# Performance work log

Hardware: AMD Instinct MI355X
Metric: run time of the kernel (lower is better)

## Reference

```python
import jax, jax.numpy as jnp
import numpy as np

N_NODES = 50000
N_EDGES = 800000


def _sage(x, src, dst, Wl, bl, Wr):
    # mean-aggregate neighbor features (messages flow src -> dst), then linear
    msg = x[src]                                              # [E, d_in]
    s = jax.ops.segment_sum(msg, dst, num_segments=N_NODES)   # [N, d_in]
    cnt = jax.ops.segment_sum(jnp.ones((src.shape[0],), x.dtype), dst,
                              num_segments=N_NODES)           # [N]
    agg = s / jnp.maximum(cnt, 1.0)[:, None]
    return agg @ Wl.T + bl + x @ Wr.T


def setup_inputs() -> dict:
    key = jax.random.key(0)
    ks = jax.random.split(key, 10)
    d_in, h = 128, 64
    def w(k, o, i):
        return jax.random.normal(k, (o, i), jnp.float32) * (1.0 / np.sqrt(i))
    return {
        "x": jax.random.normal(ks[0], (N_NODES, d_in), jnp.float32),
        "edge_index": jax.random.randint(ks[1], (2, N_EDGES), 0, N_NODES, jnp.int64),
        "Wl1": w(ks[2], h, d_in), "bl1": jnp.zeros((h,), jnp.float32), "Wr1": w(ks[3], h, d_in),
        "Wl2": w(ks[4], 2 * h, h), "bl2": jnp.zeros((2 * h,), jnp.float32), "Wr2": w(ks[5], 2 * h, h),
        "Wl3": w(ks[6], 2 * h, 2 * h), "bl3": jnp.zeros((2 * h,), jnp.float32), "Wr3": w(ks[7], 2 * h, 2 * h),
        "Wl4": w(ks[8], h, 2 * h), "bl4": jnp.zeros((h,), jnp.float32), "Wr4": w(ks[9], h, 2 * h),
    }


def reference(x, edge_index, Wl1, bl1, Wr1, Wl2, bl2, Wr2, Wl3, bl3, Wr3, Wl4, bl4, Wr4):
    src, dst = edge_index[0], edge_index[1]
    h = jax.nn.relu(_sage(x, src, dst, Wl1, bl1, Wr1))
    h = jax.nn.relu(_sage(h, src, dst, Wl2, bl2, Wr2))
    h = jax.nn.relu(_sage(h, src, dst, Wl3, bl3, Wr3))
    h = _sage(h, src, dst, Wl4, bl4, Wr4)
    return h
```

## Files before the change

kernel.cpp:

```cpp
#include <hip/hip_runtime.h>

#define NN 50000
#define NE 800000
#define GB 391
#define NBUK 196
#define PB 128
#define CH 6250
#define HLEN (NBUK * PB)
#define SAB (HLEN / 256)

typedef __attribute__((ext_vector_type(8))) short short8v;
typedef __attribute__((ext_vector_type(4))) float float4v;

__device__ __forceinline__ int uni(int v) { return __builtin_amdgcn_readfirstlane(v); }
__device__ __forceinline__ unsigned short f2bf(float f) {
    unsigned u = __float_as_uint(f);
    return (unsigned short)((u + 0x7FFFu + ((u >> 16) & 1u)) >> 16);
}
__device__ __forceinline__ float bf2f(unsigned short h) {
    return __uint_as_float(((unsigned)h) << 16);
}

__global__ __launch_bounds__(256) void hist_kernel(const int* __restrict__ dst,
                                                   int* __restrict__ H) {
    __shared__ int h[NBUK];
    const int t = threadIdx.x;
    const int b = blockIdx.x;
    if (t < NBUK) h[t] = 0;
    __syncthreads();
    const int e0 = b * CH;
    for (int i = t; i < CH; i += 256) {
        int e = e0 + i;
        if (e < NE) atomicAdd(&h[dst[e] >> 8], 1);
    }
    __syncthreads();
    if (t < NBUK) H[t * PB + b] = h[t];
}

__global__ __launch_bounds__(256) void scanA_kernel(const int* __restrict__ a,
                                                    int* __restrict__ part) {
    __shared__ int red[256];
    const int t = threadIdx.x;
    red[t] = a[blockIdx.x * 256 + t];
    __syncthreads();
#pragma unroll
    for (int d = 128; d > 0; d >>= 1) {
        if (t < d) red[t] += red[t + d];
        __syncthreads();
    }
    if (t == 0) part[blockIdx.x] = red[0];
}

__global__ __launch_bounds__(128) void scanB_kernel(int* __restrict__ part) {
    __shared__ int ps[128];
    const int t = threadIdx.x;
    ps[t] = (t < SAB) ? part[t] : 0;
    __syncthreads();
#pragma unroll
    for (int d = 1; d < 128; d <<= 1) {
        int v = (t >= d) ? ps[t - d] : 0;
        __syncthreads();
        ps[t] += v;
        __syncthreads();
    }
    if (t < SAB) part[t] = (t == 0) ? 0 : ps[t - 1];
}

__global__ __launch_bounds__(256) void scanC_kernel(int* __restrict__ a,
                                                    const int* __restrict__ part) {
    __shared__ int ps[256];
    const int t = threadIdx.x;
    const int i = blockIdx.x * 256 + t;
    const int c = a[i];
    ps[t] = c;
    __syncthreads();
#pragma unroll
    for (int d = 1; d < 256; d <<= 1) {
        int v = (t >= d) ? ps[t - d] : 0;
        __syncthreads();
        ps[t] += v;
        __syncthreads();
    }
    a[i] = part[blockIdx.x] + ps[t] - c;
}

__global__ __launch_bounds__(256) void partition_kernel(const int* __restrict__ src,
                                                        const int* __restrict__ dst,
                                                        const int* __restrict__ Hs,
                                                        unsigned* __restrict__ tmp) {
    __shared__ int cur[NBUK];
    const int t = threadIdx.x;
    const int b = blockIdx.x;
    if (t < NBUK) cur[t] = Hs[t * PB + b];
    __syncthreads();
    const int e0 = b * CH;
    for (int i = t; i < CH; i += 256) {
        int e = e0 + i;
        if (e < NE) {
            const int d = dst[e];
            const int k = d >> 8;
            const int pos = atomicAdd(&cur[k], 1);
            tmp[pos] = (unsigned)src[e] | ((unsigned)(d & 255) << 16);
        }
    }
}

__global__ __launch_bounds__(256) void finalize_kernel(const unsigned* __restrict__ tmp,
                                                       const int* __restrict__ Hs,
                                                       int* __restrict__ off,
                                                       int* __restrict__ cnt,
                                                       float* __restrict__ inv,
                                                       int* __restrict__ srcs) {
    __shared__ int hist[256];
    __shared__ int ps[256];
    __shared__ int cur[256];
    const int t = threadIdx.x;
    const int k = blockIdx.x;
    const int s0 = Hs[k * PB];
    const int end = (k == NBUK - 1) ? NE : Hs[(k + 1) * PB];
    const int m = end - s0;
    hist[t] = 0;
    __syncthreads();
    for (int i = t; i < m; i += 256) {
        atomicAdd(&hist[(tmp[s0 + i] >> 16) & 255], 1);
    }
    __syncthreads();
    const int c = hist[t];
    ps[t] = c;
    __syncthreads();
#pragma unroll
    for (int d = 1; d < 256; d <<= 1) {
        int v = (t >= d) ? ps[t - d] : 0;
        __syncthreads();
        ps[t] += v;
        __syncthreads();
    }
    const int ex = ps[t] - c;
    const int node = k * 256 + t;
    if (node < NN) {
        off[node] = s0 + ex;
        cnt[node] = c;
        inv[node] = 1.0f / (float)max(c, 1);
    }
    cur[t] = s0 + ex;
    __syncthreads();
    for (int i = t; i < m; i += 256) {
        const unsigned u = tmp[s0 + i];
        const int p = atomicAdd(&cur[(u >> 16) & 255], 1);
        srcs[p] = (int)(u & 0xFFFFu);
    }
}

template<int D, int MODE, int DUALB>
__global__ __launch_bounds__(256) void gather_kernel(
    const unsigned short* __restrict__ yb, int ys, const int* __restrict__ srcs,
    const int* __restrict__ off, const int* __restrict__ cnt,
    const float* __restrict__ inv, const float* __restrict__ pre, int ps,
    float* __restrict__ out, int os, unsigned short* __restrict__ outb) {
    const int w = (blockIdx.x * blockDim.x + threadIdx.x) >> 6;
    const int lane = threadIdx.x & 63;
    if (w >= NN) return;
    const int o = uni(off[w]);
    const int n = uni(cnt[w]);
    const int h = lane >> 5;
    const int l = lane & 31;

    float a0 = 0.0f, a1 = 0.0f, a2 = 0.0f, a3 = 0.0f;
    int i = 0;
    for (; i + 8 <= n; i += 8) {
        int e0 = srcs[o + i + h];
        int e1 = srcs[o + i + 2 + h];
        int e2 = srcs[o + i + 4 + h];
        int e3 = srcs[o + i + 6 + h];
        if constexpr (D == 64) {
            const ushort2 v0 = *reinterpret_cast<const ushort2*>(&yb[(size_t)e0 * ys + 2 * l]);
            const ushort2 v1 = *reinterpret_cast<const ushort2*>(&yb[(size_t)e1 * ys + 2 * l]);
            const ushort2 v2 = *reinterpret_cast<const ushort2*>(&yb[(size_t)e2 * ys + 2 * l]);
            const ushort2 v3 = *reinterpret_cast<const ushort2*>(&yb[(size_t)e3 * ys + 2 * l]);
            a0 += bf2f(v0.x) + bf2f(v1.x) + bf2f(v2.x) + bf2f(v3.x);
            a1 += bf2f(v0.y) + bf2f(v1.y) + bf2f(v2.y) + bf2f(v3.y);
        } else {
            const ushort4 v0 = *reinterpret_cast<const ushort4*>(&yb[(size_t)e0 * ys + 4 * l]);
            const ushort4 v1 = *reinterpret_cast<const ushort4*>(&yb[(size_t)e1 * ys + 4 * l]);
            const ushort4 v2 = *reinterpret_cast<const ushort4*>(&yb[(size_t)e2 * ys + 4 * l]);
            const ushort4 v3 = *reinterpret_cast<const ushort4*>(&yb[(size_t)e3 * ys + 4 * l]);
            a0 += bf2f(v0.x) + bf2f(v1.x) + bf2f(v2.x) + bf2f(v3.x);
            a1 += bf2f(v0.y) + bf2f(v1.y) + bf2f(v2.y) + bf2f(v3.y);
            a2 += bf2f(v0.z) + bf2f(v1.z) + bf2f(v2.z) + bf2f(v3.z);
            a3 += bf2f(v0.w) + bf2f(v1.w) + bf2f(v2.w) + bf2f(v3.w);
        }
    }
    for (; i + 2 <= n; i += 2) {
        int e = srcs[o + i + h];
        if constexpr (D == 64) {
            const ushort2 v = *reinterpret_cast<const ushort2*>(&yb[(size_t)e * ys + 2 * l]);
            a0 += bf2f(v.x);
            a1 += bf2f(v.y);
        } else {
            const ushort4 v = *reinterpret_cast<const ushort4*>(&yb[(size_t)e * ys + 4 * l]);
            a0 += bf2f(v.x); a1 += bf2f(v.y); a2 += bf2f(v.z); a3 += bf2f(v.w);
        }
    }
    if (i < n && h == 0) {
        int e = srcs[o + i];
        if constexpr (D == 64) {
            const ushort2 v = *reinterpret_cast<const ushort2*>(&yb[(size_t)e * ys + 2 * l]);
            a0 += bf2f(v.x);
            a1 += bf2f(v.y);
        } else {
            const ushort4 v = *reinterpret_cast<const ushort4*>(&yb[(size_t)e * ys + 4 * l]);
            a0 += bf2f(v.x); a1 += bf2f(v.y); a2 += bf2f(v.z); a3 += bf2f(v.w);
        }
    }
    a0 += __shfl_xor(a0, 32, 64);
    a1 += __shfl_xor(a1, 32, 64);
    if constexpr (D == 128) {
        a2 += __shfl_xor(a2, 32, 64);
        a3 += __shfl_xor(a3, 32, 64);
    }
    if (h != 0) return;

    const float iv = inv[w];
    if constexpr (D == 64) {
        float r0 = a0 * iv, r1 = a1 * iv;
        if constexpr (MODE != 0) {
            const float2 pv = *reinterpret_cast<const float2*>(&pre[(size_t)w * ps + 2 * l]);
            r0 += pv.x; r1 += pv.y;
        }
        if constexpr (MODE == 1) { r0 = fmaxf(r0, 0.0f); r1 = fmaxf(r1, 0.0f); }
        float2 sv = {r0, r1};
        *reinterpret_cast<float2*>(&out[(size_t)w * os + 2 * l]) = sv;
        if constexpr (DUALB) {
            ushort2 bv = {f2bf(r0), f2bf(r1)};
            *reinterpret_cast<ushort2*>(&outb[(size_t)w * 64 + 2 * l]) = bv;
        }
    } else {
        float r0 = a0 * iv, r1 = a1 * iv, r2 = a2 * iv, r3 = a3 * iv;
        if constexpr (MODE != 0) {
            const float4 pv = *reinterpret_cast<const float4*>(&pre[(size_t)w * ps + 4 * l]);
            r0 += pv.x; r1 += pv.y; r2 += pv.z; r3 += pv.w;
        }
        if constexpr (MODE == 1) {
            r0 = fmaxf(r0, 0.0f); r1 = fmaxf(r1, 0.0f);
            r2 = fmaxf(r2, 0.0f); r3 = fmaxf(r3, 0.0f);
        }
        float4 sv = {r0, r1, r2, r3};
        *reinterpret_cast<float4*>(&out[(size_t)w * os + 4 * l]) = sv;
    }
}

struct WSrc { const float* p[8]; };

__global__ __launch_bounds__(256) void wplanes_kernel(WSrc S,
                                                      unsigned short* __restrict__ ph,
                                                      unsigned short* __restrict__ pl) {
    const int e = blockIdx.x * 256 + threadIdx.x;
    const int seg = blockIdx.y;
    const int row = e >> 7, k = e & 127;
    float x;
    switch (seg) {
        case 0:  x = (row < 64) ? S.p[0][row * 128 + k] : S.p[1][(row - 64) * 128 + k]; break;
        case 1:  x = (k < 64)   ? S.p[2][row * 64 + k]  : S.p[3][row * 64 + (k - 64)];  break;
        case 2:  x = S.p[4][e]; break;
        case 3:  x = S.p[5][e]; break;
        default: x = (row < 64) ? S.p[6][row * 128 + k] : S.p[7][(row - 64) * 128 + k]; break;
    }
    const unsigned u = __float_as_uint(x);
    const float lo = x - __uint_as_float(u & 0xFFFF0000u);
    const int o = seg * 16384 + e;
    ph[o] = (unsigned short)(u >> 16);
    pl[o] = (unsigned short)(__float_as_uint(lo) >> 16);
}

__global__ __launch_bounds__(256) void gemm_mfma(
    const float* __restrict__ in,
    const unsigned short* __restrict__ Bh, const unsigned short* __restrict__ Bl,
    float* __restrict__ out0, const float* __restrict__ bias0, int os0, int obf0,
    float* __restrict__ out1, const float* __restrict__ bias1, int os1, int obf1,
    int relu) {
    const int t = threadIdx.x;
    const int lane = t & 63;
    const int wid = t >> 6;
    const int wn = wid & 1;
    const int wc = wid >> 1;
    const int l15 = lane & 15;
    const int lk = lane >> 4;
    const int nb = (int)blockIdx.x * 128 + wn * 64;

    float* const outp = wc ? out1 : out0;
    const float* const biasp = wc ? bias1 : bias0;
    const int os = wc ? os1 : os0;
    const int obf = wc ? obf1 : obf0;
    const unsigned short* const Bhp = Bh + (size_t)(wc * 64) * 128;
    const unsigned short* const Blp = Bl + (size_t)(wc * 64) * 128;
    const ptrdiff_t dlo = Blp - Bhp;

    float4v acc[4][4];
#pragma unroll
    for (int mi = 0; mi < 4; ++mi)
#pragma unroll
        for (int ci = 0; ci < 4; ++ci) acc[mi][ci] = (float4v)0.0f;

    const float* arow[4];
#pragma unroll
    for (int mi = 0; mi < 4; ++mi) {
        int r = nb + mi * 16 + l15;
        if (r > NN - 1) r = NN - 1;
        arow[mi] = in + (size_t)r * 128;
    }
    const unsigned short* brow[4];
#pragma unroll
    for (int ci = 0; ci < 4; ++ci) brow[ci] = Bhp + (size_t)(ci * 16 + l15) * 128;

    for (int ks = 0; ks < 4; ++ks) {
        const int ko = ks * 32 + lk * 8;
        short8v Ah[4], Al[4];
#pragma unroll
        for (int mi = 0; mi < 4; ++mi) {
            const float4v v0 = *reinterpret_cast<const float4v*>(arow[mi] + ko);
            const float4v v1 = *reinterpret_cast<const float4v*>(arow[mi] + ko + 4);
            float xv[8] = {v0.x, v0.y, v0.z, v0.w, v1.x, v1.y, v1.z, v1.w};
            union { unsigned u[4]; short8v s; } H, L;
#pragma unroll
            for (int q = 0; q < 4; ++q) {
                const unsigned u0 = __float_as_uint(xv[2 * q]);
                const unsigned u1 = __float_as_uint(xv[2 * q + 1]);
                const float l0 = xv[2 * q]     - __uint_as_float(u0 & 0xFFFF0000u);
                const float l1 = xv[2 * q + 1] - __uint_as_float(u1 & 0xFFFF0000u);
                H.u[q] = (u1 & 0xFFFF0000u) | (u0 >> 16);
                L.u[q] = (__float_as_uint(l1) & 0xFFFF0000u) | (__float_as_uint(l0) >> 16);
            }
            Ah[mi] = H.s;
            Al[mi] = L.s;
        }
        short8v Bhf[4], Blf[4];
#pragma unroll
        for (int ci = 0; ci < 4; ++ci) {
            Bhf[ci] = *reinterpret_cast<const short8v*>(brow[ci] + ko);
            Blf[ci] = *reinterpret_cast<const short8v*>(brow[ci] + dlo + ko);
        }
#pragma unroll
        for (int mi = 0; mi < 4; ++mi)
#pragma unroll
            for (int ci = 0; ci < 4; ++ci) {
                acc[mi][ci] = __builtin_amdgcn_mfma_f32_16x16x32_bf16(Ah[mi], Bhf[ci], acc[mi][ci], 0, 0, 0);
                acc[mi][ci] = __builtin_amdgcn_mfma_f32_16x16x32_bf16(Ah[mi], Blf[ci], acc[mi][ci], 0, 0, 0);
                acc[mi][ci] = __builtin_amdgcn_mfma_f32_16x16x32_bf16(Al[mi], Bhf[ci], acc[mi][ci], 0, 0, 0);
            }
    }

#pragma unroll
    for (int ci = 0; ci < 4; ++ci) {
        const int c = ci * 16 + l15;
        const float b = biasp ? biasp[c] : 0.0f;
#pragma unroll
        for (int mi = 0; mi < 4; ++mi) {
#pragma unroll
            for (int j = 0; j < 4; ++j) {
                const int r = nb + mi * 16 + lk * 4 + j;
                if (r < NN) {
                    float v = acc[mi][ci][j] + b;
                    if (relu) v = fmaxf(v, 0.0f);
                    if (obf) ((unsigned short*)outp)[(size_t)r * os + c] = f2bf(v);
                    else outp[(size_t)r * os + c] = v;
                }
            }
        }
    }
}

extern "C" void kernel_launch(void* const* d_in, const int* in_sizes, int n_in,
                              void* d_out, int out_size, void* d_ws, size_t ws_size,
                              hipStream_t stream) {
    const float* x   = (const float*)d_in[0];
    const int*   eix = (const int*)d_in[1];
    const float* Wl1 = (const float*)d_in[2];
    const float* bl1 = (const float*)d_in[3];
    const float* Wr1 = (const float*)d_in[4];
    const float* Wl2 = (const float*)d_in[5];
    const float* bl2 = (const float*)d_in[6];
    const float* Wr2 = (const float*)d_in[7];
    const float* Wl3 = (const float*)d_in[8];
    const float* bl3 = (const float*)d_in[9];
    const float* Wr3 = (const float*)d_in[10];
    const float* Wl4 = (const float*)d_in[11];
    const float* bl4 = (const float*)d_in[12];
    const float* Wr4 = (const float*)d_in[13];
    float* out = (float*)d_out;

    const int* src = eix;
    const int* dst = eix + NE;

    char* ws = (char*)d_ws;
    int*   cnt  = (int*)ws;
    int*   off  = cnt + NN;
    float* inv  = (float*)(off + NN);
    int*   Hs   = (int*)(inv + NN);
    int*   part = Hs + HLEN;
    int*   srcs = part + 256;
    unsigned short* ph = (unsigned short*)(srcs + NE);
    unsigned short* pl = ph + 81920;
    unsigned short* XB1 = pl + 81920;
    unsigned short* H1B = XB1 + (size_t)NN * 64;
    unsigned short* G3B = XB1;
    float* HCAT = (float*)(XB1 + (size_t)NN * 128);
    float* H2   = HCAT + (size_t)NN * 128;
    float* HPRE = H2 + (size_t)NN * 128;
    unsigned*       tmp = (unsigned*)HPRE;
    unsigned short* G4B = (unsigned short*)HCAT;

    hist_kernel<<<PB, 256, 0, stream>>>(dst, Hs);
    scanA_kernel<<<SAB, 256, 0, stream>>>(Hs, part);
    scanB_kernel<<<1, 128, 0, stream>>>(part);
    scanC_kernel<<<SAB, 256, 0, stream>>>(Hs, part);
    partition_kernel<<<PB, 256, 0, stream>>>(src, dst, Hs, tmp);
    finalize_kernel<<<NBUK, 256, 0, stream>>>(tmp, Hs, off, cnt, inv, srcs);

    {
        WSrc s;
        s.p[0] = Wl1; s.p[1] = Wr1; s.p[2] = Wl2; s.p[3] = Wr2;
        s.p[4] = Wl3; s.p[5] = Wr3; s.p[6] = Wl4; s.p[7] = Wr4;
        wplanes_kernel<<<dim3(64, 5), 256, 0, stream>>>(s, ph, pl);
    }

    gemm_mfma<<<GB, 256, 0, stream>>>(x, ph, pl,
                                      (float*)XB1, nullptr, 64, 1,
                                      HCAT + 64, bl1, 128, 0, 0);
    gather_kernel<64, 1, 1><<<12500, 256, 0, stream>>>(
        XB1, 64, srcs, off, cnt, inv, HCAT + 64, 128, HCAT + 64, 128, H1B);

    gather_kernel<64, 0, 0><<<12500, 256, 0, stream>>>(
        H1B, 64, srcs, off, cnt, inv, nullptr, 0, HCAT, 128, nullptr);
    gemm_mfma<<<GB, 256, 0, stream>>>(HCAT, ph + 16384, pl + 16384,
                                      H2, bl2, 128, 0,
                                      H2 + 64, bl2 + 64, 128, 0, 1);

    gemm_mfma<<<GB, 256, 0, stream>>>(H2, ph + 2 * 16384, pl + 2 * 16384,
                                      (float*)G3B, nullptr, 128, 1,
                                      (float*)(G3B + 64), nullptr, 128, 1, 0);
    gemm_mfma<<<GB, 256, 0, stream>>>(H2, ph + 3 * 16384, pl + 3 * 16384,
                                      HPRE, bl3, 128, 0,
                                      HPRE + 64, bl3 + 64, 128, 0, 0);
    gather_kernel<128, 1, 0><<<12500, 256, 0, stream>>>(
        G3B, 128, srcs, off, cnt, inv, HPRE, 128, HPRE, 128, nullptr);

    gemm_mfma<<<GB, 256, 0, stream>>>(HPRE, ph + 4 * 16384, pl + 4 * 16384,
                                      (float*)G4B, nullptr, 64, 1,
                                      out, bl4, 64, 0, 0);
    gather_kernel<64, 2, 0><<<12500, 256, 0, stream>>>(
        G4B, 64, srcs, off, cnt, inv, out, 64, out, 64, nullptr);
}
```

Before: 323.9 us.

## Use 16-bit edge indices, nontemporal memory ops, and merge layer-3 GEMM launches

Stores the CSR source index array as 16-bit values to halve index bandwidth in the gather kernels. Adds nontemporal loads and stores across the gather and GEMM kernels to reduce cache pollution. Merges the two layer-3 GEMMs that share an input into a single launch using a 2D grid with per-y argument structs. Nontemporal stores of intermediates that are read right afterwards may lose L2 reuse, and the 16-bit index relies on node count staying below 65536.

```diff
diff --git a/kernel.cpp b/kernel.cpp
--- a/kernel.cpp
+++ b/kernel.cpp
@@ -11,6 +11,8 @@
 
 typedef __attribute__((ext_vector_type(8))) short short8v;
 typedef __attribute__((ext_vector_type(4))) float float4v;
+typedef __attribute__((ext_vector_type(2))) float float2v;
+typedef __attribute__((ext_vector_type(2))) unsigned short ushort2v;
 
 __device__ __forceinline__ int uni(int v) { return __builtin_amdgcn_readfirstlane(v); }
 __device__ __forceinline__ unsigned short f2bf(float f) {
@@ -110,7 +112,7 @@
                                                        int* __restrict__ off,
                                                        int* __restrict__ cnt,
                                                        float* __restrict__ inv,
-                                                       int* __restrict__ srcs) {
+                                                       unsigned short* __restrict__ srcs) {
     __shared__ int hist[256];
     __shared__ int ps[256];
     __shared__ int cur[256];
@@ -147,13 +149,13 @@
     for (int i = t; i < m; i += 256) {
         const unsigned u = tmp[s0 + i];
         const int p = atomicAdd(&cur[(u >> 16) & 255], 1);
-        srcs[p] = (int)(u & 0xFFFFu);
+        srcs[p] = (unsigned short)(u & 0xFFFFu);
     }
 }
 
 template<int D, int MODE, int DUALB>
 __global__ __launch_bounds__(256) void gather_kernel(
-    const unsigned short* __restrict__ yb, int ys, const int* __restrict__ srcs,
+    const unsigned short* __restrict__ yb, int ys, const unsigned short* __restrict__ srcs,
     const int* __restrict__ off, const int* __restrict__ cnt,
     const float* __restrict__ inv, const float* __restrict__ pre, int ps,
     float* __restrict__ out, int os, unsigned short* __restrict__ outb) {
@@ -168,10 +170,10 @@
     float a0 = 0.0f, a1 = 0.0f, a2 = 0.0f, a3 = 0.0f;
     int i = 0;
     for (; i + 8 <= n; i += 8) {
-        int e0 = srcs[o + i + h];
-        int e1 = srcs[o + i + 2 + h];
-        int e2 = srcs[o + i + 4 + h];
-        int e3 = srcs[o + i + 6 + h];
+        int e0 = __builtin_nontemporal_load(&srcs[o + i + h]);
+        int e1 = __builtin_nontemporal_load(&srcs[o + i + 2 + h]);
+        int e2 = __builtin_nontemporal_load(&srcs[o + i + 4 + h]);
+        int e3 = __builtin_nontemporal_load(&srcs[o + i + 6 + h]);
         if constexpr (D == 64) {
             const ushort2 v0 = *reinterpret_cast<const ushort2*>(&yb[(size_t)e0 * ys + 2 * l]);
             const ushort2 v1 = *reinterpret_cast<const ushort2*>(&yb[(size_t)e1 * ys + 2 * l]);
@@ -191,7 +193,7 @@
         }
     }
     for (; i + 2 <= n; i += 2) {
-        int e = srcs[o + i + h];
+        int e = __builtin_nontemporal_load(&srcs[o + i + h]);
         if constexpr (D == 64) {
             const ushort2 v = *reinterpret_cast<const ushort2*>(&yb[(size_t)e * ys + 2 * l]);
             a0 += bf2f(v.x);
@@ -202,7 +204,7 @@
         }
     }
     if (i < n && h == 0) {
-        int e = srcs[o + i];
+        int e = __builtin_nontemporal_load(&srcs[o + i]);
         if constexpr (D == 64) {
             const ushort2 v = *reinterpret_cast<const ushort2*>(&yb[(size_t)e * ys + 2 * l]);
             a0 += bf2f(v.x);
@@ -224,28 +226,30 @@
     if constexpr (D == 64) {
         float r0 = a0 * iv, r1 = a1 * iv;
         if constexpr (MODE != 0) {
-            const float2 pv = *reinterpret_cast<const float2*>(&pre[(size_t)w * ps + 2 * l]);
+            const float2v pv = __builtin_nontemporal_load(
+                reinterpret_cast<const float2v*>(&pre[(size_t)w * ps + 2 * l]));
             r0 += pv.x; r1 += pv.y;
         }
         if constexpr (MODE == 1) { r0 = fmaxf(r0, 0.0f); r1 = fmaxf(r1, 0.0f); }
-        float2 sv = {r0, r1};
-        *reinterpret_cast<float2*>(&out[(size_t)w * os + 2 * l]) = sv;
+        float2v sv = {r0, r1};
+        __builtin_nontemporal_store(sv, reinterpret_cast<float2v*>(&out[(size_t)w * os + 2 * l]));
         if constexpr (DUALB) {
-            ushort2 bv = {f2bf(r0), f2bf(r1)};
-            *reinterpret_cast<ushort2*>(&outb[(size_t)w * 64 + 2 * l]) = bv;
+            ushort2v bv = {f2bf(r0), f2bf(r1)};
+            __builtin_nontemporal_store(bv, reinterpret_cast<ushort2v*>(&outb[(size_t)w * 64 + 2 * l]));
         }
     } else {
         float r0 = a0 * iv, r1 = a1 * iv, r2 = a2 * iv, r3 = a3 * iv;
         if constexpr (MODE != 0) {
-            const float4 pv = *reinterpret_cast<const float4*>(&pre[(size_t)w * ps + 4 * l]);
+            const float4v pv = __builtin_nontemporal_load(
+                reinterpret_cast<const float4v*>(&pre[(size_t)w * ps + 4 * l]));
             r0 += pv.x; r1 += pv.y; r2 += pv.z; r3 += pv.w;
         }
         if constexpr (MODE == 1) {
             r0 = fmaxf(r0, 0.0f); r1 = fmaxf(r1, 0.0f);
             r2 = fmaxf(r2, 0.0f); r3 = fmaxf(r3, 0.0f);
         }
-        float4 sv = {r0, r1, r2, r3};
-        *reinterpret_cast<float4*>(&out[(size_t)w * os + 4 * l]) = sv;
+        float4v sv = {r0, r1, r2, r3};
+        __builtin_nontemporal_store(sv, reinterpret_cast<float4v*>(&out[(size_t)w * os + 4 * l]));
     }
 }
 
@@ -272,12 +276,16 @@
     pl[o] = (unsigned short)(__float_as_uint(lo) >> 16);
 }
 
-__global__ __launch_bounds__(256) void gemm_mfma(
-    const float* __restrict__ in,
-    const unsigned short* __restrict__ Bh, const unsigned short* __restrict__ Bl,
-    float* __restrict__ out0, const float* __restrict__ bias0, int os0, int obf0,
-    float* __restrict__ out1, const float* __restrict__ bias1, int os1, int obf1,
-    int relu) {
+struct GemmArgs {
+    const unsigned short* Bh; const unsigned short* Bl;
+    float* out0; const float* bias0; int os0, obf0;
+    float* out1; const float* bias1; int os1, obf1;
+    int relu;
+};
+
+__global__ __launch_bounds__(256) void gemm_mfma(const float* __restrict__ in,
+                                                 GemmArgs A0, GemmArgs A1) {
+    const GemmArgs G = blockIdx.y ? A1 : A0;
     const int t = threadIdx.x;
     const int lane = t & 63;
     const int wid = t >> 6;
@@ -287,12 +295,12 @@
     const int lk = lane >> 4;
     const int nb = (int)blockIdx.x * 128 + wn * 64;
 
-    float* const outp = wc ? out1 : out0;
-    const float* const biasp = wc ? bias1 : bias0;
-    const int os = wc ? os1 : os0;
-    const int obf = wc ? obf1 : obf0;
-    const unsigned short* const Bhp = Bh + (size_t)(wc * 64) * 128;
-    const unsigned short* const Blp = Bl + (size_t)(wc * 64) * 128;
+    float* const outp = wc ? G.out1 : G.out0;
+    const float* const biasp = wc ? G.bias1 : G.bias0;
+    const int os = wc ? G.os1 : G.os0;
+    const int obf = wc ? G.obf1 : G.obf0;
+    const unsigned short* const Bhp = G.Bh + (size_t)(wc * 64) * 128;
+    const unsigned short* const Blp = G.Bl + (size_t)(wc * 64) * 128;
     const ptrdiff_t dlo = Blp - Bhp;
 
     float4v acc[4][4];
@@ -317,8 +325,10 @@
         short8v Ah[4], Al[4];
 #pragma unroll
         for (int mi = 0; mi < 4; ++mi) {
-            const float4v v0 = *reinterpret_cast<const float4v*>(arow[mi] + ko);
-            const float4v v1 = *reinterpret_cast<const float4v*>(arow[mi] + ko + 4);
+            const float4v v0 = __builtin_nontemporal_load(
+                reinterpret_cast<const float4v*>(arow[mi] + ko));
+            const float4v v1 = __builtin_nontemporal_load(
+                reinterpret_cast<const float4v*>(arow[mi] + ko + 4));
             float xv[8] = {v0.x, v0.y, v0.z, v0.w, v1.x, v1.y, v1.z, v1.w};
             union { unsigned u[4]; short8v s; } H, L;
 #pragma unroll
@@ -360,9 +370,13 @@
                 const int r = nb + mi * 16 + lk * 4 + j;
                 if (r < NN) {
                     float v = acc[mi][ci][j] + b;
-                    if (relu) v = fmaxf(v, 0.0f);
-                    if (obf) ((unsigned short*)outp)[(size_t)r * os + c] = f2bf(v);
-                    else outp[(size_t)r * os + c] = v;
+                    if (G.relu) v = fmaxf(v, 0.0f);
+                    if (obf) {
+                        __builtin_nontemporal_store(
+                            f2bf(v), &((unsigned short*)outp)[(size_t)r * os + c]);
+                    } else {
+                        __builtin_nontemporal_store(v, &outp[(size_t)r * os + c]);
+                    }
                 }
             }
         }
@@ -397,8 +411,8 @@
     float* inv  = (float*)(off + NN);
     int*   Hs   = (int*)(inv + NN);
     int*   part = Hs + HLEN;
-    int*   srcs = part + 256;
-    unsigned short* ph = (unsigned short*)(srcs + NE);
+    unsigned short* srcs = (unsigned short*)(part + 256);
+    unsigned short* ph = srcs + NE;
     unsigned short* pl = ph + 81920;
     unsigned short* XB1 = pl + 81920;
     unsigned short* H1B = XB1 + (size_t)NN * 64;
@@ -423,30 +437,37 @@
         wplanes_kernel<<<dim3(64, 5), 256, 0, stream>>>(s, ph, pl);
     }
 
-    gemm_mfma<<<GB, 256, 0, stream>>>(x, ph, pl,
-                                      (float*)XB1, nullptr, 64, 1,
-                                      HCAT + 64, bl1, 128, 0, 0);
+    {
+        GemmArgs a{ph, pl, (float*)XB1, nullptr, 64, 1, HCAT + 64, bl1, 128, 0, 0};
+        gemm_mfma<<<dim3(GB, 1), 256, 0, stream>>>(x, a, a);
+    }
     gather_kernel<64, 1, 1><<<12500, 256, 0, stream>>>(
         XB1, 64, srcs, off, cnt, inv, HCAT + 64, 128, HCAT + 64, 128, H1B);
 
     gather_kernel<64, 0, 0><<<12500, 256, 0, stream>>>(
         H1B, 64, srcs, off, cnt, inv, nullptr, 0, HCAT, 128, nullptr);
-    gemm_mfma<<<GB, 256, 0, stream>>>(HCAT, ph + 16384, pl + 16384,
-                                      H2, bl2, 128, 0,
-                                      H2 + 64, bl2 + 64, 128, 0, 1);
-
-    gemm_mfma<<<GB, 256, 0, stream>>>(H2, ph + 2 * 16384, pl + 2 * 16384,
-                                      (float*)G3B, nullptr, 128, 1,
-                                      (float*)(G3B + 64), nullptr, 128, 1, 0);
-    gemm_mfma<<<GB, 256, 0, stream>>>(H2, ph + 3 * 16384, pl + 3 * 16384,
-                                      HPRE, bl3, 128, 0,
-                                      HPRE + 64, bl3 + 64, 128, 0, 0);
+    {
+        GemmArgs a{ph + 16384, pl + 16384, H2, bl2, 128, 0, H2 + 64, bl2 + 64, 128, 0, 1};
+        gemm_mfma<<<dim3(GB, 1), 256, 0, stream>>>(HCAT, a, a);
+    }
+
+    {
+        GemmArgs a0{ph + 2 * 16384, pl + 2 * 16384,
+                    (float*)G3B, nullptr, 128, 1,
+                    (float*)(G3B + 64), nullptr, 128, 1, 0};
+        GemmArgs a1{ph + 3 * 16384, pl + 3 * 16384,
+                    HPRE, bl3, 128, 0,
+                    HPRE + 64, bl3 + 64, 128, 0, 0};
+        gemm_mfma<<<dim3(GB, 2), 256, 0, stream>>>(H2, a0, a1);
+    }
     gather_kernel<128, 1, 0><<<12500, 256, 0, stream>>>(
         G3B, 128, srcs, off, cnt, inv, HPRE, 128, HPRE, 128, nullptr);
 
-    gemm_mfma<<<GB, 256, 0, stream>>>(HPRE, ph + 4 * 16384, pl + 4 * 16384,
-                                      (float*)G4B, nullptr, 64, 1,
-                                      out, bl4, 64, 0, 0);
+    {
+        GemmArgs a{ph + 4 * 16384, pl + 4 * 16384,
+                   (float*)G4B, nullptr, 64, 1, out, bl4, 64, 0, 0};
+        gemm_mfma<<<dim3(GB, 1), 256, 0, stream>>>(HPRE, a, a);
+    }
     gather_kernel<64, 2, 0><<<12500, 256, 0, stream>>>(
         G4B, 64, srcs, off, cnt, inv, out, 64, out, 64, nullptr);
 }
```

Result: slower. 395.6 us (+22.1%).
